# Kernel tuning notes

Hardware: AMD Instinct MI355X
Metric: run time of the kernel (lower is better)

The kernel has to match this reference:

```python
import jax, jax.numpy as jnp
import numpy as np

R = 32768          # rays
S = 128            # fixed step budget per ray (padded/masked)
STEP = 0.02        # step_size
NX = NY = NZ = 256
MINB = jnp.array([-1.0, -1.0, -1.0], jnp.float32)
MAXB = jnp.array([1.0, 1.0, 1.0], jnp.float32)
# voxel sizes: (max - min) / (n - 1)
VOX = (MAXB - MINB) / (jnp.array([NX, NY, NZ], jnp.float32) - 1.0)
N = jnp.array([NX, NY, NZ], jnp.int32)
# 8 corner offsets, same order as the original query_voxels
OFFS = jnp.array([[0,0,0],[1,0,0],[0,1,0],[1,1,0],
                  [0,0,1],[1,0,1],[0,1,1],[1,1,1]], jnp.int32)


def setup_inputs() -> dict:
    key = jax.random.key(0)
    k1, k2, k3 = jax.random.split(key, 3)
    origins = jax.random.uniform(k1, (R, 3), jnp.float32, -0.9, 0.9)
    d = jax.random.normal(k2, (R, 3), jnp.float32)
    directions = d / jnp.linalg.norm(d, axis=-1, keepdims=True)
    sdf_values = jax.random.normal(k3, (NX, NY, NZ), jnp.float32)
    return {"origins": origins, "directions": directions, "sdf_values": sdf_values}


def reference(origins, directions, sdf_values):
    # --- ray_box_intersection (faithful, including the tmin reuse in tmax) ---
    inv_dir = 1.0 / directions                       # [R,3]
    a = (MINB - origins) * inv_dir                   # [R,3]
    b = (MAXB - origins) * inv_dir                   # [R,3]
    t0 = jnp.max(jnp.minimum(a, b), axis=-1)         # [R] scalar tmin
    t1 = jnp.min(jnp.maximum(t0[:, None], b), axis=-1)  # [R] (original overwrites tmin first)
    hit = t1 >= t0                                   # original returns None if tmax < tmin

    # --- march_ray: fixed step grid t = t_near + i*step, masked at t >= t_far ---
    t = t0[:, None] + STEP * jnp.arange(S, dtype=jnp.float32)   # [R,S]
    step_mask = (t < t1[:, None]) & hit[:, None]                # [R,S]
    pts = origins[:, None, :] + t[..., None] * directions[:, None, :]  # [R,S,3]

    # --- query_voxels: truncating index like torch .long() ---
    idx = ((pts - MINB) / VOX).astype(jnp.int32)                # [R,S,3]
    inb = jnp.all((idx >= 0) & (idx < N - 1), axis=-1)          # [R,S]
    valid = inb & step_mask                                     # [R,S]
    idxc = jnp.clip(idx, 0, N - 2)                              # safe gather indices
    ci = idxc[:, :, None, :] + OFFS                             # [R,S,8,3]
    sdf = sdf_values[ci[..., 0], ci[..., 1], ci[..., 2]]        # [R,S,8] 8-corner gather
    sdf = jnp.where(valid[..., None], sdf, 0.0)
    positions = MINB + ci.astype(jnp.float32) * VOX             # [R,S,8,3] corner positions
    positions = jnp.where(valid[..., None, None], positions, 0.0)
    return sdf, positions, valid
```

## Files before the change

### kernel.cpp

```cpp
#include <hip/hip_runtime.h>


constexpr int   RAYS = 32768;
constexpr int   STEPS = 128;
constexpr float STEP = 0.02f;
constexpr float VOX = 2.0f / 255.0f;

typedef float f4 __attribute__((ext_vector_type(4)));
typedef float f2 __attribute__((ext_vector_type(2), aligned(4)));

__global__ __launch_bounds__(256) void sdf_march_kernel(
    const float* __restrict__ org,
    const float* __restrict__ dir,
    const float* __restrict__ sdfv,
    float* __restrict__ out_sdf,
    float* __restrict__ out_pos,
    float* __restrict__ out_valid)
{
#pragma clang fp contract(off)
    __shared__ f4 lds_pos[1536];
    __shared__ f4 lds_sdf[512];

    const int tid = threadIdx.x;
    const int gid = blockIdx.x * 256 + tid;
    const int r = gid >> 7;
    const int s = gid & 127;

    const float ox = org[r * 3 + 0], oy = org[r * 3 + 1], oz = org[r * 3 + 2];
    const float dx = dir[r * 3 + 0], dy = dir[r * 3 + 1], dz = dir[r * 3 + 2];

    const float ivx = 1.0f / dx, ivy = 1.0f / dy, ivz = 1.0f / dz;
    const float axv = (-1.0f - ox) * ivx, ayv = (-1.0f - oy) * ivy, azv = (-1.0f - oz) * ivz;
    const float bxv = ( 1.0f - ox) * ivx, byv = ( 1.0f - oy) * ivy, bzv = ( 1.0f - oz) * ivz;
    const float t0 = fmaxf(fmaxf(fminf(axv, bxv), fminf(ayv, byv)), fminf(azv, bzv));
    const float t1 = fminf(fminf(fmaxf(t0, bxv), fmaxf(t0, byv)), fmaxf(t0, bzv));
    const bool hit = (t1 >= t0);

    const float ts = STEP * (float)s;
    const float t  = t0 + ts;
    const bool step_mask = (t < t1) && hit;

    const float mx = t * dx, my = t * dy, mz = t * dz;
    const float px = ox + mx, py = oy + my, pz = oz + mz;

    const float fx = (px + 1.0f) / VOX;
    const float fy = (py + 1.0f) / VOX;
    const float fz = (pz + 1.0f) / VOX;
    const int ix = (int)fx, iy = (int)fy, iz = (int)fz;
    const bool inb = (ix >= 0) & (ix < 255) & (iy >= 0) & (iy < 255) & (iz >= 0) & (iz < 255);
    const bool valid = inb && step_mask;

    const int ixc = min(max(ix, 0), 254);
    const int iyc = min(max(iy, 0), 254);
    const int izc = min(max(iz, 0), 254);

    f2 vz00 = {0.f, 0.f}, vz10 = {0.f, 0.f}, vz01 = {0.f, 0.f}, vz11 = {0.f, 0.f};
    if (valid) {
        const int base = (ixc * 256 + iyc) * 256 + izc;
        vz00 = *(const f2*)(sdfv + base);
        vz10 = *(const f2*)(sdfv + base + 65536);
        vz01 = *(const f2*)(sdfv + base + 256);
        vz11 = *(const f2*)(sdfv + base + 65536 + 256);
    }

    float x0 = 0.f, x1 = 0.f, y0 = 0.f, y1 = 0.f, z0 = 0.f, z1 = 0.f;
    if (valid) {
        x0 = -1.0f + (float)ixc * VOX;
        x1 = -1.0f + (float)(ixc + 1) * VOX;
        y0 = -1.0f + (float)iyc * VOX;
        y1 = -1.0f + (float)(iyc + 1) * VOX;
        z0 = -1.0f + (float)izc * VOX;
        z1 = -1.0f + (float)(izc + 1) * VOX;
    }

    f4* lp = lds_pos + tid * 6;
    lp[0] = (f4){x0, y0, z0, x1};
    lp[1] = (f4){y0, z0, x0, y1};
    lp[2] = (f4){z0, x1, y1, z0};
    lp[3] = (f4){x0, y0, z1, x1};
    lp[4] = (f4){y0, z1, x0, y1};
    lp[5] = (f4){z1, x1, y1, z1};

    __builtin_nontemporal_store(valid ? 1.0f : 0.0f, out_valid + gid);

    __syncthreads();

    f4* op = (f4*)out_pos + (size_t)blockIdx.x * 1536;
#pragma unroll
    for (int k = 0; k < 6; ++k) {
        __builtin_nontemporal_store(lds_pos[tid + 256 * k], op + tid + 256 * k);
    }

    const f4 sv0 = (f4){vz00.x, vz10.x, vz01.x, vz11.x};
    const f4 sv1 = (f4){vz00.y, vz10.y, vz01.y, vz11.y};
    lds_sdf[tid * 2 + 0] = sv0;
    lds_sdf[tid * 2 + 1] = sv1;

    __syncthreads();

    f4* os = (f4*)out_sdf + (size_t)blockIdx.x * 512;
    __builtin_nontemporal_store(lds_sdf[tid],       os + tid);
    __builtin_nontemporal_store(lds_sdf[tid + 256], os + tid + 256);
}

extern "C" void kernel_launch(void* const* d_in, const int* in_sizes, int n_in,
                              void* d_out, int out_size, void* d_ws, size_t ws_size,
                              hipStream_t stream) {
    const float* origins    = (const float*)d_in[0];
    const float* directions = (const float*)d_in[1];
    const float* sdf_values = (const float*)d_in[2];

    float* out = (float*)d_out;
    float* out_sdf   = out;
    float* out_pos   = out + 33554432;
    float* out_valid = out + 33554432 + 100663296;

    const int total = RAYS * STEPS;
    dim3 grid(total / 256), block(256);
    sdf_march_kernel<<<grid, block, 0, stream>>>(origins, directions, sdf_values,
                                                 out_sdf, out_pos, out_valid);
}
```

Baseline: 592.8 us.

## Split position and SDF outputs into separate block roles

Launches twice as many blocks. The first half writes the corner positions and the valid flags, and the second half gathers the SDF corners and writes them. Both halves recompute the ray setup. The split shrinks LDS per block to one shared buffer and separates the store-heavy work from the gather-heavy work, so more blocks can be resident and the gather latency can overlap with position stores. The cost is the ray math and index computation done twice, plus a doubled grid.

```diff
diff --git a/kernel.cpp b/kernel.cpp
--- a/kernel.cpp
+++ b/kernel.cpp
@@ -5,6 +5,7 @@
 constexpr int   STEPS = 128;
 constexpr float STEP = 0.02f;
 constexpr float VOX = 2.0f / 255.0f;
+constexpr int   NBLK = (RAYS * STEPS) / 256;
 
 typedef float f4 __attribute__((ext_vector_type(4)));
 typedef float f2 __attribute__((ext_vector_type(2), aligned(4)));
@@ -18,13 +19,14 @@
     float* __restrict__ out_valid)
 {
 #pragma clang fp contract(off)
-    __shared__ f4 lds_pos[1536];
-    __shared__ f4 lds_sdf[512];
+    __shared__ f4 lds[1536];
 
-    const int tid = threadIdx.x;
-    const int gid = blockIdx.x * 256 + tid;
-    const int r = gid >> 7;
-    const int s = gid & 127;
+    const int  tid     = threadIdx.x;
+    const bool posRole = (blockIdx.x < NBLK);
+    const int  rb      = posRole ? blockIdx.x : (blockIdx.x - NBLK);
+    const int  gid     = rb * 256 + tid;
+    const int  r = gid >> 7;
+    const int  s = gid & 127;
 
     const float ox = org[r * 3 + 0], oy = org[r * 3 + 1], oz = org[r * 3 + 2];
     const float dx = dir[r * 3 + 0], dy = dir[r * 3 + 1], dz = dir[r * 3 + 2];
@@ -54,53 +56,51 @@
     const int iyc = min(max(iy, 0), 254);
     const int izc = min(max(iz, 0), 254);
 
-    f2 vz00 = {0.f, 0.f}, vz10 = {0.f, 0.f}, vz01 = {0.f, 0.f}, vz11 = {0.f, 0.f};
-    if (valid) {
-        const int base = (ixc * 256 + iyc) * 256 + izc;
-        vz00 = *(const f2*)(sdfv + base);
-        vz10 = *(const f2*)(sdfv + base + 65536);
-        vz01 = *(const f2*)(sdfv + base + 256);
-        vz11 = *(const f2*)(sdfv + base + 65536 + 256);
+    if (posRole) {
+        float x0 = 0.f, x1 = 0.f, y0 = 0.f, y1 = 0.f, z0 = 0.f, z1 = 0.f;
+        if (valid) {
+            x0 = -1.0f + (float)ixc * VOX;
+            x1 = -1.0f + (float)(ixc + 1) * VOX;
+            y0 = -1.0f + (float)iyc * VOX;
+            y1 = -1.0f + (float)(iyc + 1) * VOX;
+            z0 = -1.0f + (float)izc * VOX;
+            z1 = -1.0f + (float)(izc + 1) * VOX;
+        }
+        f4* lp = lds + tid * 6;
+        lp[0] = (f4){x0, y0, z0, x1};
+        lp[1] = (f4){y0, z0, x0, y1};
+        lp[2] = (f4){z0, x1, y1, z0};
+        lp[3] = (f4){x0, y0, z1, x1};
+        lp[4] = (f4){y0, z1, x0, y1};
+        lp[5] = (f4){z1, x1, y1, z1};
+
+        __builtin_nontemporal_store(valid ? 1.0f : 0.0f, out_valid + gid);
+
+        __syncthreads();
+
+        f4* op = (f4*)out_pos + (size_t)rb * 1536;
+#pragma unroll
+        for (int k = 0; k < 6; ++k) {
+            __builtin_nontemporal_store(lds[tid + 256 * k], op + tid + 256 * k);
+        }
+    } else {
+        f2 vz00 = {0.f, 0.f}, vz10 = {0.f, 0.f}, vz01 = {0.f, 0.f}, vz11 = {0.f, 0.f};
+        if (valid) {
+            const int base = (ixc * 256 + iyc) * 256 + izc;
+            vz00 = *(const f2*)(sdfv + base);
+            vz10 = *(const f2*)(sdfv + base + 65536);
+            vz01 = *(const f2*)(sdfv + base + 256);
+            vz11 = *(const f2*)(sdfv + base + 65536 + 256);
+        }
+        lds[tid * 2 + 0] = (f4){vz00.x, vz10.x, vz01.x, vz11.x};
+        lds[tid * 2 + 1] = (f4){vz00.y, vz10.y, vz01.y, vz11.y};
+
+        __syncthreads();
+
+        f4* os = (f4*)out_sdf + (size_t)rb * 512;
+        __builtin_nontemporal_store(lds[tid],       os + tid);
+        __builtin_nontemporal_store(lds[tid + 256], os + tid + 256);
     }
-
-    float x0 = 0.f, x1 = 0.f, y0 = 0.f, y1 = 0.f, z0 = 0.f, z1 = 0.f;
-    if (valid) {
-        x0 = -1.0f + (float)ixc * VOX;
-        x1 = -1.0f + (float)(ixc + 1) * VOX;
-        y0 = -1.0f + (float)iyc * VOX;
-        y1 = -1.0f + (float)(iyc + 1) * VOX;
-        z0 = -1.0f + (float)izc * VOX;
-        z1 = -1.0f + (float)(izc + 1) * VOX;
-    }
-
-    f4* lp = lds_pos + tid * 6;
-    lp[0] = (f4){x0, y0, z0, x1};
-    lp[1] = (f4){y0, z0, x0, y1};
-    lp[2] = (f4){z0, x1, y1, z0};
-    lp[3] = (f4){x0, y0, z1, x1};
-    lp[4] = (f4){y0, z1, x0, y1};
-    lp[5] = (f4){z1, x1, y1, z1};
-
-    __builtin_nontemporal_store(valid ? 1.0f : 0.0f, out_valid + gid);
-
-    __syncthreads();
-
-    f4* op = (f4*)out_pos + (size_t)blockIdx.x * 1536;
-#pragma unroll
-    for (int k = 0; k < 6; ++k) {
-        __builtin_nontemporal_store(lds_pos[tid + 256 * k], op + tid + 256 * k);
-    }
-
-    const f4 sv0 = (f4){vz00.x, vz10.x, vz01.x, vz11.x};
-    const f4 sv1 = (f4){vz00.y, vz10.y, vz01.y, vz11.y};
-    lds_sdf[tid * 2 + 0] = sv0;
-    lds_sdf[tid * 2 + 1] = sv1;
-
-    __syncthreads();
-
-    f4* os = (f4*)out_sdf + (size_t)blockIdx.x * 512;
-    __builtin_nontemporal_store(lds_sdf[tid],       os + tid);
-    __builtin_nontemporal_store(lds_sdf[tid + 256], os + tid + 256);
 }
 
 extern "C" void kernel_launch(void* const* d_in, const int* in_sizes, int n_in,
@@ -115,8 +115,7 @@
     float* out_pos   = out + 33554432;
     float* out_valid = out + 33554432 + 100663296;
 
-    const int total = RAYS * STEPS;
-    dim3 grid(total / 256), block(256);
+    dim3 grid(2 * NBLK), block(256);
     sdf_march_kernel<<<grid, block, 0, stream>>>(origins, directions, sdf_values,
                                                  out_sdf, out_pos, out_valid);
 }
```

New measurement: 599.1 us. No clear change (+1.1%).
